# Optimization experiments

Hardware: AMD Instinct MI355X
Metric: run time of the kernel (lower is better)

Reference implementation:

```python
import jax, jax.numpy as jnp
import numpy as np

C = 512
G = 2  # num_groups in Normalize default
EPS = 1e-6


def setup_inputs() -> dict:
    key = jax.random.key(0)
    ks = jax.random.split(key, 11)
    B, H, W = 4, 64, 64
    s = 1.0 / np.sqrt(C)
    return {
        "x": jax.random.normal(ks[0], (B, C, H, W), dtype=jnp.float32),
        "gn_w": jnp.ones((C,), jnp.float32),
        "gn_b": jnp.zeros((C,), jnp.float32),
        "wq": jax.random.normal(ks[1], (C, C), jnp.float32) * s,
        "bq": jnp.zeros((C,), jnp.float32),
        "wk": jax.random.normal(ks[2], (C, C), jnp.float32) * s,
        "bk": jnp.zeros((C,), jnp.float32),
        "wv": jax.random.normal(ks[3], (C, C), jnp.float32) * s,
        "bv": jnp.zeros((C,), jnp.float32),
        "wp": jax.random.normal(ks[4], (C, C), jnp.float32) * s,
        "bp": jnp.zeros((C,), jnp.float32),
    }


def _group_norm(x, w, b):
    # x: [B, C, H, W]; GroupNorm over (C//G, H, W) within each group
    B, Cc, H, Wd = x.shape
    xg = x.reshape(B, G, Cc // G, H, Wd)
    mu = jnp.mean(xg, axis=(2, 3, 4), keepdims=True)
    var = jnp.var(xg, axis=(2, 3, 4), keepdims=True)
    xn = (xg - mu) * jax.lax.rsqrt(var + EPS)
    xn = xn.reshape(B, Cc, H, Wd)
    return xn * w[None, :, None, None] + b[None, :, None, None]


def _conv1x1(x, w, b):
    # 1x1 conv == channel matmul. x: [B,C,H,W], w: [O,C]
    return jnp.einsum('bchw,oc->bohw', x, w) + b[None, :, None, None]


def reference(x, gn_w, gn_b, wq, bq, wk, bk, wv, bv, wp, bp):
    B, Cc, H, Wd = x.shape
    h_ = _group_norm(x, gn_w, gn_b)
    q = _conv1x1(h_, wq, bq).reshape(B, Cc, H * Wd)  # [B,C,N]
    k = _conv1x1(h_, wk, bk).reshape(B, Cc, H * Wd)
    v = _conv1x1(h_, wv, bv).reshape(B, Cc, H * Wd)
    # scores: q^T k, scaled by sqrt(C) (NOTE: faithful to source, which
    # multiplies by c**0.5 instead of dividing)
    scale = jnp.sqrt(jnp.float32(Cc)).astype(x.dtype)
    attn = jnp.einsum('bcn,bcm->bnm', q, k) * scale  # [B,N,N]
    attn = jax.nn.softmax(attn, axis=2)
    # h_[b,c,n] = sum_m attn[b,n,m] * v[b,c,m]
    out = jnp.einsum('bnm,bcm->bcn', attn, v).reshape(B, Cc, H, Wd)
    out = _conv1x1(out, wp, bp)
    return x + out
```

## Files before the change

### kernel.cpp

```cpp
#include <hip/hip_runtime.h>
#include <hip/hip_bf16.h>
#include <math.h>

#define B_ 4
#define C_ 512
#define N_ 4096

typedef float f32x4 __attribute__((ext_vector_type(4)));
typedef __bf16 bf16x8 __attribute__((ext_vector_type(8)));

#define AS1(p) ((const __attribute__((address_space(1))) unsigned int*)(p))
#define AS3(p) ((__attribute__((address_space(3))) unsigned int*)(p))

__device__ __forceinline__ unsigned short f2bf(float x){
    return __builtin_bit_cast(unsigned short, (__bf16)x);
}
__device__ __forceinline__ float bf2f(unsigned short b){
    unsigned u = ((unsigned)b)<<16;
    return __builtin_bit_cast(float, u);
}
__device__ __forceinline__ f32x4 mfma16(bf16x8 a, bf16x8 b, f32x4 c){
    return __builtin_amdgcn_mfma_f32_16x16x32_bf16(a, b, c, 0, 0, 0);
}
__device__ __forceinline__ void bar_lgkm(){
    asm volatile("s_waitcnt lgkmcnt(0)" ::: "memory");
    __builtin_amdgcn_s_barrier();
}
__device__ __forceinline__ void bar_vm(){
    asm volatile("s_waitcnt vmcnt(0)" ::: "memory");
    __builtin_amdgcn_s_barrier();
}

__global__ void split_w(const float* __restrict__ src, unsigned short* __restrict__ hi,
                        unsigned short* __restrict__ lo){
    const int i = (blockIdx.x*256 + threadIdx.x)*4;
    f32x4 v = *(const f32x4*)(src + i);
    ushort4 h, l;
    unsigned short t0=f2bf(v[0]); h.x=t0; l.x=f2bf(v[0]-bf2f(t0));
    unsigned short t1=f2bf(v[1]); h.y=t1; l.y=f2bf(v[1]-bf2f(t1));
    unsigned short t2=f2bf(v[2]); h.z=t2; l.z=f2bf(v[2]-bf2f(t2));
    unsigned short t3=f2bf(v[3]); h.w=t3; l.w=f2bf(v[3]-bf2f(t3));
    *(ushort4*)(hi + i) = h;
    *(ushort4*)(lo + i) = l;
}

__global__ void gn_part(const float* __restrict__ x, float2* __restrict__ part){
    const int bg = blockIdx.y, blk = blockIdx.x, t = threadIdx.x;
    const float* base = x + (size_t)bg*(256*4096) + (size_t)blk*16384;
    float s = 0.f, q = 0.f;
    for (int i=0;i<16;i++){
        f32x4 v = *(const f32x4*)(base + i*1024 + t*4);
        s += v[0]+v[1]+v[2]+v[3];
        q += v[0]*v[0]+v[1]*v[1]+v[2]*v[2]+v[3]*v[3];
    }
    #pragma unroll
    for (int o=32;o>0;o>>=1){ s += __shfl_down(s, o); q += __shfl_down(q, o); }
    __shared__ float as[4], aq[4];
    if ((t&63)==0){ as[t>>6]=s; aq[t>>6]=q; }
    __syncthreads();
    if (t==0)
        part[bg*64 + blk] = make_float2(as[0]+as[1]+as[2]+as[3], aq[0]+aq[1]+aq[2]+aq[3]);
}

__global__ void gn_fin(const float2* __restrict__ part, float2* __restrict__ stats){
    const int bg = blockIdx.x, t = threadIdx.x;
    float2 p = part[bg*64 + t];
    float s = p.x, q = p.y;
    #pragma unroll
    for (int o=32;o>0;o>>=1){ s += __shfl_down(s,o); q += __shfl_down(q,o); }
    if (t==0){
        const float inv = 1.0f/(256.f*4096.f);
        float mu = s*inv;
        float var = q*inv - mu*mu;
        stats[bg] = make_float2(mu, rsqrtf(var + 1e-6f));
    }
}

__global__ void gn_apply(const float* __restrict__ x, const float* __restrict__ gw,
                         const float* __restrict__ gb, const float2* __restrict__ stats,
                         unsigned short* __restrict__ hTh, unsigned short* __restrict__ hTl)
{
    const int b = blockIdx.z, c0 = blockIdx.y*32, n0 = blockIdx.x*32;
    const int t = threadIdx.x;
    __shared__ float tile[32][37];
    {
        const int cl = t>>3, nl = (t&7)*4;
        const int c = c0 + cl;
        const float2 st = stats[b*2 + (c>>8)];
        const float wv = gw[c], bvv = gb[c];
        const f32x4 v = *(const f32x4*)(x + ((size_t)b*C_ + c)*N_ + n0 + nl);
        #pragma unroll
        for (int i=0;i<4;i++) tile[cl][nl+i] = (v[i] - st.x)*st.y*wv + bvv;
    }
    __syncthreads();
    {
        const int nl = t>>3, cl = (t&7)*4;
        const int n = n0 + nl;
        float f0 = tile[cl+0][nl], f1 = tile[cl+1][nl], f2 = tile[cl+2][nl], f3 = tile[cl+3][nl];
        unsigned short h0=f2bf(f0), h1=f2bf(f1), h2=f2bf(f2), h3=f2bf(f3);
        ushort4 hh, ll;
        hh.x=h0; hh.y=h1; hh.z=h2; hh.w=h3;
        ll.x=f2bf(f0-bf2f(h0)); ll.y=f2bf(f1-bf2f(h1));
        ll.z=f2bf(f2-bf2f(h2)); ll.w=f2bf(f3-bf2f(h3));
        size_t o = ((size_t)b*N_ + n)*C_ + c0 + cl;
        *(ushort4*)(hTh + o) = hh;
        *(ushort4*)(hTl + o) = ll;
    }
}

template<int PROD, int MODE>
__global__ __launch_bounds__(256, 2) void conv_gemm(
    const unsigned short* __restrict__ Wh, const unsigned short* __restrict__ Wl,
    const unsigned short* __restrict__ Sh, const unsigned short* __restrict__ Sl,
    const float* __restrict__ bias,
    unsigned short* __restrict__ outHi, unsigned short* __restrict__ outLo,
    float* __restrict__ outF, const float* __restrict__ resid)
{
    const int b = blockIdx.z, o0 = blockIdx.y*128, n0 = blockIdx.x*128;
    const int t = threadIdx.x, w = t>>6, l = t&63, lr = l&15, lg = l>>4;
    const int ro = (w>>1)*64, co = (w&1)*64;
    __shared__ unsigned short Ah[128][40];
    __shared__ unsigned short Al[128][40];
    __shared__ unsigned short Bh[128][40];
    __shared__ unsigned short Bl[128][40];
    f32x4 acc[4][4];
    #pragma unroll
    for (int i=0;i<4;i++)
        #pragma unroll
        for (int j=0;j<4;j++) acc[i][j] = (f32x4){0.f,0.f,0.f,0.f};

    const size_t srcB = (size_t)b*N_*C_;
    for (int ks=0; ks<16; ks++){
        const int c0 = ks*32;
        #pragma unroll
        for (int i=0;i<2;i++){
            int u = t + i*256;
            int row = u>>2, sch = (u&3)*8;
            *(bf16x8*)&Ah[row][sch] = *(const bf16x8*)(Wh + (size_t)(o0+row)*C_ + c0 + sch);
            *(bf16x8*)&Bh[row][sch] = *(const bf16x8*)(Sh + srcB + (size_t)(n0+row)*C_ + c0 + sch);
            if constexpr (PROD==3){
                *(bf16x8*)&Al[row][sch] = *(const bf16x8*)(Wl + (size_t)(o0+row)*C_ + c0 + sch);
                *(bf16x8*)&Bl[row][sch] = *(const bf16x8*)(Sl + srcB + (size_t)(n0+row)*C_ + c0 + sch);
            }
        }
        __syncthreads();
        bf16x8 af[4], bfv[4], afl[4], bfl[4];
        #pragma unroll
        for (int i=0;i<4;i++){
            af[i]  = *(const bf16x8*)&Ah[ro + i*16 + lr][lg*8];
            bfv[i] = *(const bf16x8*)&Bh[co + i*16 + lr][lg*8];
            if constexpr (PROD==3){
                afl[i] = *(const bf16x8*)&Al[ro + i*16 + lr][lg*8];
                bfl[i] = *(const bf16x8*)&Bl[co + i*16 + lr][lg*8];
            }
        }
        #pragma unroll
        for (int i=0;i<4;i++)
            #pragma unroll
            for (int j=0;j<4;j++){
                acc[i][j] = mfma16(af[i], bfv[j], acc[i][j]);
                if constexpr (PROD==3){
                    acc[i][j] = mfma16(af[i],  bfl[j], acc[i][j]);
                    acc[i][j] = mfma16(afl[i], bfv[j], acc[i][j]);
                }
            }
        __syncthreads();
    }
    #pragma unroll
    for (int i=0;i<4;i++){
        const int ob = o0 + ro + i*16 + lg*4;
        #pragma unroll
        for (int j=0;j<4;j++){
            const int n = n0 + co + j*16 + lr;
            f32x4 v = acc[i][j];
            if constexpr (MODE==0){
                float v0 = v[0] + bias[ob+0]; unsigned short h0 = f2bf(v0);
                float v1 = v[1] + bias[ob+1]; unsigned short h1 = f2bf(v1);
                float v2 = v[2] + bias[ob+2]; unsigned short h2 = f2bf(v2);
                float v3 = v[3] + bias[ob+3]; unsigned short h3 = f2bf(v3);
                ushort4 hh, ll;
                hh.x=h0; hh.y=h1; hh.z=h2; hh.w=h3;
                ll.x=f2bf(v0-bf2f(h0)); ll.y=f2bf(v1-bf2f(h1));
                ll.z=f2bf(v2-bf2f(h2)); ll.w=f2bf(v3-bf2f(h3));
                *(ushort4*)(outHi + srcB + (size_t)n*C_ + ob) = hh;
                *(ushort4*)(outLo + srcB + (size_t)n*C_ + ob) = ll;
            } else if constexpr (MODE==1){
                #pragma unroll
                for (int r=0;r<4;r++)
                    outHi[((size_t)b*C_ + ob + r)*N_ + n] = f2bf(v[r] + bias[ob+r]);
            } else {
                #pragma unroll
                for (int r=0;r<4;r++){
                    size_t idx = ((size_t)b*C_ + ob + r)*N_ + n;
                    outF[idx] = resid[idx] + v[r] + bias[ob+r];
                }
            }
        }
    }
}

__global__ __launch_bounds__(512, 2) void attn_flash3(
    const unsigned short* __restrict__ qTh, const unsigned short* __restrict__ qTl,
    const unsigned short* __restrict__ kTh, const unsigned short* __restrict__ kTl,
    const unsigned short* __restrict__ vB,  unsigned short* __restrict__ aoT)
{
    const int b = blockIdx.y, n0 = blockIdx.x*64;
    const int t = threadIdx.x, w = t>>6, l = t&63, lr = l&15, lg = l>>4;
    const int fm2 = w>>2, fn = (w>>1)&1, ch = w&1;
    const int cw = w*64;

    __shared__ unsigned short khA[32*512];
    __shared__ unsigned short klA[32*512];
    __shared__ unsigned short khB[32*512];
    __shared__ unsigned short klB[32*512];
    __shared__ float Sb[2][64][34];
    __shared__ __align__(16) unsigned short Pb[64][40];
    __shared__ float rowM[64], rowS[64], rowF[64];

    bf16x8 qh[2][8], ql[2][8];
    #pragma unroll
    for (int f=0; f<2; f++){
        const size_t qr = ((size_t)b*N_ + n0 + fm2*32 + f*16 + lr)*C_ + ch*256;
        #pragma unroll
        for (int kc=0; kc<8; kc++){
            qh[f][kc] = *(const bf16x8*)(qTh + qr + kc*32 + lg*8);
            ql[f][kc] = *(const bf16x8*)(qTl + qr + kc*32 + lg*8);
        }
    }
    f32x4 accO[4][4];
    #pragma unroll
    for (int i=0;i<4;i++)
        #pragma unroll
        for (int j=0;j<4;j++) accO[i][j] = (f32x4){0.f,0.f,0.f,0.f};
    if (t < 64){ rowM[t] = -INFINITY; rowS[t] = 0.f; rowF[t] = 1.f; }

    const size_t kBase = (size_t)b*N_*1024;

    auto stage = [&](int mt, unsigned short* dh, unsigned short* dl){
        const size_t kb = kBase + (size_t)mt*32*1024;
        #pragma unroll
        for (int i=0;i<4;i++){
            const int d = i*8192 + t*16;
            const int row = i*8 + w;
            const int colb = (l*16) ^ ((row&7)<<4);
            const size_t g = kb + (size_t)row*1024 + colb;
            __builtin_amdgcn_global_load_lds(AS1((const char*)kTh + g), AS3((char*)dh + d), 16, 0, 0);
            __builtin_amdgcn_global_load_lds(AS1((const char*)kTl + g), AS3((char*)dl + d), 16, 0, 0);
        }
    };

    stage(0, khA, klA);
    bar_vm();

    for (int mt=0; mt<128; mt++){
        const int cur = mt & 1;
        const unsigned short* kh = cur ? khB : khA;
        const unsigned short* kl = cur ? klB : klA;

        bf16x8 vf[4];
        {
            const size_t vcol = (size_t)mt*32 + lg*8;
            #pragma unroll
            for (int ac=0;ac<4;ac++)
                vf[ac] = *(const bf16x8*)(vB + ((size_t)b*C_ + cw + ac*16 + lr)*N_ + vcol);
        }

        f32x4 s0 = (f32x4){0.f,0.f,0.f,0.f}, s1 = s0;
        {
            const int krow = fn*16 + lr;
            const int rbase = krow*1024;
            const int swz = (krow&7)<<4;
            #pragma unroll
            for (int kc=0;kc<8;kc++){
                const int o = rbase + ((ch*512 + kc*64 + lg*16) ^ swz);
                bf16x8 kf  = *(const bf16x8*)((const char*)kh + o);
                bf16x8 kfl = *(const bf16x8*)((const char*)kl + o);
                s0 = mfma16(qh[0][kc], kf,  s0);
                s0 = mfma16(ql[0][kc], kf,  s0);
                s0 = mfma16(qh[0][kc], kfl, s0);
                s1 = mfma16(qh[1][kc], kf,  s1);
                s1 = mfma16(ql[1][kc], kf,  s1);
                s1 = mfma16(qh[1][kc], kfl, s1);
            }
        }
        #pragma unroll
        for (int r=0;r<4;r++){
            Sb[ch][fm2*32 +      lg*4 + r][fn*16 + lr] = s0[r];
            Sb[ch][fm2*32 + 16 + lg*4 + r][fn*16 + lr] = s1[r];
        }
        if (mt < 127) stage(mt+1, cur ? khA : khB, cur ? klA : klB);
        bar_lgkm();

        {
            const int row = t>>3, j = t&7;
            const float* p0v = &Sb[0][row][j*4];
            const float* p1v = &Sb[1][row][j*4];
            float2 u0 = *(const float2*)p0v, u1 = *(const float2*)(p0v+2);
            float2 w0 = *(const float2*)p1v, w1 = *(const float2*)(p1v+2);
            const float SC = 22.62741699796952f;
            float a0 = (u0.x + w0.x)*SC, a1 = (u0.y + w0.y)*SC;
            float a2 = (u1.x + w1.x)*SC, a3 = (u1.y + w1.y)*SC;
            float mx = fmaxf(fmaxf(a0,a1), fmaxf(a2,a3));
            mx = fmaxf(mx, __shfl_xor(mx, 1, 8));
            mx = fmaxf(mx, __shfl_xor(mx, 2, 8));
            mx = fmaxf(mx, __shfl_xor(mx, 4, 8));
            const float mprev = rowM[row];
            const float mnew = fmaxf(mprev, mx);
            float p0 = __expf(a0 - mnew), p1 = __expf(a1 - mnew);
            float p2 = __expf(a2 - mnew), p3 = __expf(a3 - mnew);
            float ps = (p0+p1)+(p2+p3);
            ps += __shfl_xor(ps, 1, 8);
            ps += __shfl_xor(ps, 2, 8);
            ps += __shfl_xor(ps, 4, 8);
            ushort4 pk; pk.x=f2bf(p0); pk.y=f2bf(p1); pk.z=f2bf(p2); pk.w=f2bf(p3);
            *(ushort4*)&Pb[row][j*4] = pk;
            if (j==0){
                float f = __expf(mprev - mnew);
                rowF[row] = f;
                rowS[row] = rowS[row]*f + ps;
                rowM[row] = mnew;
            }
        }
        bar_lgkm();

        {
            float frv[4][4]; bool need = false;
            #pragma unroll
            for (int am=0;am<4;am++)
                #pragma unroll
                for (int r=0;r<4;r++){
                    frv[am][r] = rowF[am*16 + lg*4 + r];
                    need |= (frv[am][r] != 1.0f);
                }
            if (__any(need)){
                #pragma unroll
                for (int am=0;am<4;am++)
                    #pragma unroll
                    for (int ac=0;ac<4;ac++)
                        #pragma unroll
                        for (int r=0;r<4;r++) accO[am][ac][r] *= frv[am][r];
            }
            bf16x8 pa[4];
            #pragma unroll
            for (int am=0;am<4;am++) pa[am] = *(const bf16x8*)&Pb[am*16 + lr][lg*8];
            #pragma unroll
            for (int ac=0;ac<4;ac++)
                #pragma unroll
                for (int am=0;am<4;am++)
                    accO[am][ac] = mfma16(pa[am], vf[ac], accO[am][ac]);
        }
        bar_vm();
    }

    #pragma unroll
    for (int am=0;am<4;am++)
        #pragma unroll
        for (int r=0;r<4;r++){
            const int n = am*16 + lg*4 + r;
            const float inv = 1.0f / rowS[n];
            #pragma unroll
            for (int ac=0;ac<4;ac++)
                aoT[((size_t)b*N_ + n0 + n)*C_ + cw + ac*16 + lr] = f2bf(accO[am][ac][r]*inv);
        }
}

extern "C" void kernel_launch(void* const* d_in, const int* in_sizes, int n_in,
                              void* d_out, int out_size, void* d_ws, size_t ws_size,
                              hipStream_t stream)
{
    const float* x   = (const float*)d_in[0];
    const float* gnw = (const float*)d_in[1];
    const float* gnb = (const float*)d_in[2];
    const float* wq  = (const float*)d_in[3];
    const float* bq  = (const float*)d_in[4];
    const float* wk  = (const float*)d_in[5];
    const float* bk  = (const float*)d_in[6];
    const float* wv  = (const float*)d_in[7];
    const float* bv  = (const float*)d_in[8];
    const float* wp  = (const float*)d_in[9];
    const float* bp  = (const float*)d_in[10];
    float* out = (float*)d_out;

    char* ws = (char*)d_ws;
    size_t off = 0;
    auto alloc = [&](size_t bytes)->char*{
        char* p = ws + off; off += (bytes + 255) & ~(size_t)255; return p;
    };
    const size_t WB = (size_t)C_*C_*2;
    const size_t TB = (size_t)B_*N_*C_*2;
    unsigned short* wqh = (unsigned short*)alloc(WB);
    unsigned short* wql = (unsigned short*)alloc(WB);
    unsigned short* wkh = (unsigned short*)alloc(WB);
    unsigned short* wkl = (unsigned short*)alloc(WB);
    unsigned short* wvh = (unsigned short*)alloc(WB);
    unsigned short* wvl = (unsigned short*)alloc(WB);
    unsigned short* wph = (unsigned short*)alloc(WB);
    unsigned short* wpl = (unsigned short*)alloc(WB);
    unsigned short* hTh = (unsigned short*)alloc(TB);
    unsigned short* hTl = (unsigned short*)alloc(TB);
    unsigned short* qTh = (unsigned short*)alloc(TB);
    unsigned short* qTl = (unsigned short*)alloc(TB);
    unsigned short* kTh = (unsigned short*)alloc(TB);
    unsigned short* kTl = (unsigned short*)alloc(TB);
    unsigned short* vb  = (unsigned short*)alloc(TB);
    unsigned short* ao  = (unsigned short*)alloc(TB);
    float2* part  = (float2*)alloc(8*64*sizeof(float2));
    float2* stats = (float2*)alloc(8*sizeof(float2));

    split_w<<<256, 256, 0, stream>>>(wq, wqh, wql);
    split_w<<<256, 256, 0, stream>>>(wk, wkh, wkl);
    split_w<<<256, 256, 0, stream>>>(wv, wvh, wvl);
    split_w<<<256, 256, 0, stream>>>(wp, wph, wpl);
    gn_part<<<dim3(64, 8), 256, 0, stream>>>(x, part);
    gn_fin<<<8, 64, 0, stream>>>(part, stats);
    gn_apply<<<dim3(128, 16, B_), 256, 0, stream>>>(x, gnw, gnb, stats, hTh, hTl);
    conv_gemm<3,0><<<dim3(32,4,B_), 256, 0, stream>>>(wqh,wql,hTh,hTl,bq, qTh,qTl,nullptr,nullptr);
    conv_gemm<3,0><<<dim3(32,4,B_), 256, 0, stream>>>(wkh,wkl,hTh,hTl,bk, kTh,kTl,nullptr,nullptr);
    conv_gemm<1,1><<<dim3(32,4,B_), 256, 0, stream>>>(wvh,wvl,hTh,hTl,bv, vb,nullptr,nullptr,nullptr);
    attn_flash3<<<dim3(64, B_), 512, 0, stream>>>(qTh,qTl,kTh,kTl,vb,ao);
    conv_gemm<1,2><<<dim3(32,4,B_), 256, 0, stream>>>(wph,wpl,ao,nullptr,bp, nullptr,nullptr,out,x);
}
```

Measured before the change: 542.3 us.

## Software-pipeline QK and PV in flash attention, remap blocks to XCDs, swizzle P

Restructures the attention main loop so the next tile's V load and QK^T MFMA run after the current PV MFMA, with K staged two tiles ahead. The goal is to overlap softmax and memory latency with matrix work and cut barriers per iteration. It also maps blocks of the same batch onto the same XCD pair for L2 reuse of K/V, folds the scale into the score store, swizzles the P buffer to avoid LDS bank conflicts, and raises wave priority around the MFMA section. In exchange it holds more live registers (vf carried across iterations), which may spill under the 512x2 launch bound.

New measurement: 494.9 us. 1.1x faster.

```diff
diff --git a/kernel.cpp b/kernel.cpp
--- a/kernel.cpp
+++ b/kernel.cpp
@@ -21,14 +21,6 @@
 }
 __device__ __forceinline__ f32x4 mfma16(bf16x8 a, bf16x8 b, f32x4 c){
     return __builtin_amdgcn_mfma_f32_16x16x32_bf16(a, b, c, 0, 0, 0);
-}
-__device__ __forceinline__ void bar_lgkm(){
-    asm volatile("s_waitcnt lgkmcnt(0)" ::: "memory");
-    __builtin_amdgcn_s_barrier();
-}
-__device__ __forceinline__ void bar_vm(){
-    asm volatile("s_waitcnt vmcnt(0)" ::: "memory");
-    __builtin_amdgcn_s_barrier();
 }
 
 __global__ void split_w(const float* __restrict__ src, unsigned short* __restrict__ hi,
@@ -199,12 +191,15 @@
     }
 }
 
-__global__ __launch_bounds__(512, 2) void attn_flash3(
+__global__ __launch_bounds__(512, 2) void attn_flash4(
     const unsigned short* __restrict__ qTh, const unsigned short* __restrict__ qTl,
     const unsigned short* __restrict__ kTh, const unsigned short* __restrict__ kTl,
     const unsigned short* __restrict__ vB,  unsigned short* __restrict__ aoT)
 {
-    const int b = blockIdx.y, n0 = blockIdx.x*64;
+    const int id = blockIdx.x;
+    const int xcd = id & 7, slot = id >> 3;
+    const int b = xcd >> 1;
+    const int n0 = ((xcd & 1)*32 + slot)*64;
     const int t = threadIdx.x, w = t>>6, l = t&63, lr = l&15, lg = l>>4;
     const int fm2 = w>>2, fn = (w>>1)&1, ch = w&1;
     const int cw = w*64;
@@ -213,8 +208,8 @@
     __shared__ unsigned short klA[32*512];
     __shared__ unsigned short khB[32*512];
     __shared__ unsigned short klB[32*512];
-    __shared__ float Sb[2][64][34];
-    __shared__ __align__(16) unsigned short Pb[64][40];
+    __shared__ float Sb[2][64][33];
+    __shared__ __align__(16) unsigned short Pb[64*32];
     __shared__ float rowM[64], rowS[64], rowF[64];
 
     bf16x8 qh[2][8], ql[2][8];
@@ -232,7 +227,7 @@
     for (int i=0;i<4;i++)
         #pragma unroll
         for (int j=0;j<4;j++) accO[i][j] = (f32x4){0.f,0.f,0.f,0.f};
-    if (t < 64){ rowM[t] = -INFINITY; rowS[t] = 0.f; rowF[t] = 1.f; }
+    if (t < 64){ rowM[t] = -INFINITY; rowS[t] = 0.f; }
 
     const size_t kBase = (size_t)b*N_*1024;
 
@@ -248,58 +243,56 @@
             __builtin_amdgcn_global_load_lds(AS1((const char*)kTl + g), AS3((char*)dl + d), 16, 0, 0);
         }
     };
-
+    auto loadV = [&](int mt, bf16x8* vf){
+        const size_t vcol = (size_t)mt*32 + lg*8;
+        #pragma unroll
+        for (int ac=0;ac<4;ac++)
+            vf[ac] = *(const bf16x8*)(vB + ((size_t)b*C_ + cw + ac*16 + lr)*N_ + vcol);
+    };
+    const float SC = 22.62741699796952f;
+    auto qk_tile = [&](const unsigned short* kh, const unsigned short* kl){
+        f32x4 s0 = (f32x4){0.f,0.f,0.f,0.f}, s1 = s0;
+        const int krow = fn*16 + lr;
+        const int rbase = krow*1024;
+        const int swz = (krow&7)<<4;
+        #pragma unroll
+        for (int kc=0;kc<8;kc++){
+            const int o = rbase + ((ch*512 + kc*64 + lg*16) ^ swz);
+            bf16x8 kf  = *(const bf16x8*)((const char*)kh + o);
+            bf16x8 kfl = *(const bf16x8*)((const char*)kl + o);
+            s0 = mfma16(qh[0][kc], kf,  s0);
+            s0 = mfma16(ql[0][kc], kf,  s0);
+            s0 = mfma16(qh[0][kc], kfl, s0);
+            s1 = mfma16(qh[1][kc], kf,  s1);
+            s1 = mfma16(ql[1][kc], kf,  s1);
+            s1 = mfma16(qh[1][kc], kfl, s1);
+        }
+        #pragma unroll
+        for (int r=0;r<4;r++){
+            Sb[ch][fm2*32 +      lg*4 + r][fn*16 + lr] = s0[r]*SC;
+            Sb[ch][fm2*32 + 16 + lg*4 + r][fn*16 + lr] = s1[r]*SC;
+        }
+    };
+
+    bf16x8 vf[4];
+    loadV(0, vf);
     stage(0, khA, klA);
-    bar_vm();
+    asm volatile("s_waitcnt vmcnt(0) lgkmcnt(0)" ::: "memory");
+    __builtin_amdgcn_s_barrier();
+    stage(1, khB, klB);
+    qk_tile(khA, klA);
+    asm volatile("s_waitcnt lgkmcnt(0)" ::: "memory");
+    __builtin_amdgcn_s_barrier();
 
     for (int mt=0; mt<128; mt++){
-        const int cur = mt & 1;
-        const unsigned short* kh = cur ? khB : khA;
-        const unsigned short* kl = cur ? klB : klA;
-
-        bf16x8 vf[4];
-        {
-            const size_t vcol = (size_t)mt*32 + lg*8;
-            #pragma unroll
-            for (int ac=0;ac<4;ac++)
-                vf[ac] = *(const bf16x8*)(vB + ((size_t)b*C_ + cw + ac*16 + lr)*N_ + vcol);
-        }
-
-        f32x4 s0 = (f32x4){0.f,0.f,0.f,0.f}, s1 = s0;
-        {
-            const int krow = fn*16 + lr;
-            const int rbase = krow*1024;
-            const int swz = (krow&7)<<4;
-            #pragma unroll
-            for (int kc=0;kc<8;kc++){
-                const int o = rbase + ((ch*512 + kc*64 + lg*16) ^ swz);
-                bf16x8 kf  = *(const bf16x8*)((const char*)kh + o);
-                bf16x8 kfl = *(const bf16x8*)((const char*)kl + o);
-                s0 = mfma16(qh[0][kc], kf,  s0);
-                s0 = mfma16(ql[0][kc], kf,  s0);
-                s0 = mfma16(qh[0][kc], kfl, s0);
-                s1 = mfma16(qh[1][kc], kf,  s1);
-                s1 = mfma16(ql[1][kc], kf,  s1);
-                s1 = mfma16(qh[1][kc], kfl, s1);
-            }
-        }
-        #pragma unroll
-        for (int r=0;r<4;r++){
-            Sb[ch][fm2*32 +      lg*4 + r][fn*16 + lr] = s0[r];
-            Sb[ch][fm2*32 + 16 + lg*4 + r][fn*16 + lr] = s1[r];
-        }
-        if (mt < 127) stage(mt+1, cur ? khA : khB, cur ? klA : klB);
-        bar_lgkm();
-
         {
             const int row = t>>3, j = t&7;
-            const float* p0v = &Sb[0][row][j*4];
-            const float* p1v = &Sb[1][row][j*4];
-            float2 u0 = *(const float2*)p0v, u1 = *(const float2*)(p0v+2);
-            float2 w0 = *(const float2*)p1v, w1 = *(const float2*)(p1v+2);
-            const float SC = 22.62741699796952f;
-            float a0 = (u0.x + w0.x)*SC, a1 = (u0.y + w0.y)*SC;
-            float a2 = (u1.x + w1.x)*SC, a3 = (u1.y + w1.y)*SC;
+            const float* s0p = &Sb[0][row][j*4];
+            const float* s1p = &Sb[1][row][j*4];
+            float a0 = s0p[0] + s1p[0];
+            float a1 = s0p[1] + s1p[1];
+            float a2 = s0p[2] + s1p[2];
+            float a3 = s0p[3] + s1p[3];
             float mx = fmaxf(fmaxf(a0,a1), fmaxf(a2,a3));
             mx = fmaxf(mx, __shfl_xor(mx, 1, 8));
             mx = fmaxf(mx, __shfl_xor(mx, 2, 8));
@@ -313,7 +306,8 @@
             ps += __shfl_xor(ps, 2, 8);
             ps += __shfl_xor(ps, 4, 8);
             ushort4 pk; pk.x=f2bf(p0); pk.y=f2bf(p1); pk.z=f2bf(p2); pk.w=f2bf(p3);
-            *(ushort4*)&Pb[row][j*4] = pk;
+            char* pw = (char*)Pb + row*64 + ((((j>>1) + (row>>1)) & 3)<<4) + ((j&1)<<3);
+            *(ushort4*)pw = pk;
             if (j==0){
                 float f = __expf(mprev - mnew);
                 rowF[row] = f;
@@ -321,8 +315,11 @@
                 rowM[row] = mnew;
             }
         }
-        bar_lgkm();
-
+        asm volatile("s_waitcnt vmcnt(0) lgkmcnt(0)" ::: "memory");
+        __builtin_amdgcn_s_barrier();
+
+        if (mt < 126) stage(mt+2, (mt&1) ? khB : khA, (mt&1) ? klB : klA);
+        __builtin_amdgcn_s_setprio(1);
         {
             float frv[4][4]; bool need = false;
             #pragma unroll
@@ -342,14 +339,23 @@
             }
             bf16x8 pa[4];
             #pragma unroll
-            for (int am=0;am<4;am++) pa[am] = *(const bf16x8*)&Pb[am*16 + lr][lg*8];
+            for (int am=0;am<4;am++){
+                const int prow = am*16 + lr;
+                pa[am] = *(const bf16x8*)((const char*)Pb + prow*64 + (((lg + (prow>>1)) & 3)<<4));
+            }
             #pragma unroll
             for (int ac=0;ac<4;ac++)
                 #pragma unroll
                 for (int am=0;am<4;am++)
                     accO[am][ac] = mfma16(pa[am], vf[ac], accO[am][ac]);
         }
-        bar_vm();
+        if (mt < 127){
+            loadV(mt+1, vf);
+            qk_tile(((mt+1)&1) ? khB : khA, ((mt+1)&1) ? klB : klA);
+        }
+        __builtin_amdgcn_s_setprio(0);
+        asm volatile("s_waitcnt lgkmcnt(0)" ::: "memory");
+        __builtin_amdgcn_s_barrier();
     }
 
     #pragma unroll
@@ -417,6 +423,6 @@
     conv_gemm<3,0><<<dim3(32,4,B_), 256, 0, stream>>>(wqh,wql,hTh,hTl,bq, qTh,qTl,nullptr,nullptr);
     conv_gemm<3,0><<<dim3(32,4,B_), 256, 0, stream>>>(wkh,wkl,hTh,hTl,bk, kTh,kTl,nullptr,nullptr);
     conv_gemm<1,1><<<dim3(32,4,B_), 256, 0, stream>>>(wvh,wvl,hTh,hTl,bv, vb,nullptr,nullptr,nullptr);
-    attn_flash3<<<dim3(64, B_), 512, 0, stream>>>(qTh,qTl,kTh,kTl,vb,ao);
+    attn_flash4<<<dim3(256), 512, 0, stream>>>(qTh,qTl,kTh,kTl,vb,ao);
     conv_gemm<1,2><<<dim3(32,4,B_), 256, 0, stream>>>(wph,wpl,ao,nullptr,bp, nullptr,nullptr,out,x);
 }
```
